# Kernel optimization log

Hardware: AMD Instinct MI355X
Metric: run time of the kernel (lower is better)

Reference implementation:

```python
import jax, jax.numpy as jnp
import numpy as np

SMALL = 1e-7
EPS = 1e-6


def setup_inputs() -> dict:
    key = jax.random.key(0)
    k1, k2 = jax.random.split(key)
    B, C, h, w = 8, 3, 1024, 1024
    src = jax.random.normal(k1, (B, C, h, w), dtype=jnp.float32)
    # near-identity homographies so warped coords land mostly in-bounds
    H = jnp.eye(3, dtype=jnp.float32)[None] + 0.05 * jax.random.normal(k2, (B, 3, 3), dtype=jnp.float32)
    return {"src": src, "H": H}


def reference(src, H):
    B, C, h, w = src.shape
    # homogeneous pixel grid: (3, h, w) = [x, y, 1]
    xx = jnp.arange(w, dtype=jnp.float32)
    yy = jnp.arange(h, dtype=jnp.float32)
    gx, gy = jnp.meshgrid(xx, yy)  # (h, w) each
    grid = jnp.stack([gx, gy, jnp.ones_like(gx)], axis=0)  # (3, h, w)

    # per-pixel homography transform: (B,3,h,w)
    warped = jnp.einsum('bij,jhw->bihw', H, grid)
    T = warped[:, 2]  # (B,h,w)
    T = T + EPS * (1.0 - (jnp.abs(T) >= SMALL).astype(jnp.float32))
    x = warped[:, 0] / T  # (B,h,w) source x-coords
    y = warped[:, 1] / T  # (B,h,w) source y-coords

    # bilinear sample with clamped corner indices (matches torch impl)
    x0 = jnp.floor(x).astype(jnp.int32)
    y0 = jnp.floor(y).astype(jnp.int32)
    x1 = jnp.clip(x0 + 1, 0, w - 1)
    y1 = jnp.clip(y0 + 1, 0, h - 1)
    x0 = jnp.clip(x0, 0, w - 1)
    y0 = jnp.clip(y0, 0, h - 1)

    im = jnp.transpose(src, (0, 2, 3, 1))  # (B,h,w,C)
    b = jnp.arange(B, dtype=jnp.int32)[:, None, None]  # (B,1,1)
    Ia = im[b, y0, x0]  # (B,h,w,C)
    Ib = im[b, y1, x0]
    Ic = im[b, y0, x1]
    Id = im[b, y1, x1]

    x0f, x1f = x0.astype(jnp.float32), x1.astype(jnp.float32)
    y0f, y1f = y0.astype(jnp.float32), y1.astype(jnp.float32)
    wa = ((x1f - x) * (y1f - y))[..., None]
    wb = ((x1f - x) * (y - y0f))[..., None]
    wc = ((x - x0f) * (y1f - y))[..., None]
    wd = ((x - x0f) * (y - y0f))[..., None]

    out = wa * Ia + wb * Ib + wc * Ic + wd * Id  # (B,h,w,C)
    return jnp.transpose(out, (0, 3, 1, 2))  # (B,C,h,w)
```

## Files before the change

kernel.cpp:

```cpp
#include <hip/hip_runtime.h>
#include <math.h>
#include <limits.h>
#include <string.h>


#define SMALL_F 1e-7f
#define EPS_F   1e-6f
#define PX 4

typedef float v2f __attribute__((ext_vector_type(2)));

__device__ __forceinline__ int cvt_f32_i32_x86(float f) {
    if (f >= 2147483648.0f) return INT_MIN;
    return (int)f;
}

__global__ void __launch_bounds__(256)
warp_bilinear_kernel(const float* __restrict__ src, const float* __restrict__ Hm,
                     float* __restrict__ out, int B, int h, int w) {
#pragma clang fp contract(off)
    const int b  = (int)blockIdx.y & 7;
    const int y  = (int)blockIdx.y >> 3;
    const int tx = threadIdx.x;
    const int xstart = blockIdx.x * (256 * PX) + tx;

    const float* Hb = Hm + (size_t)b * 9;
    const float H0 = Hb[0], H1 = Hb[1], H2 = Hb[2];
    const float H3 = Hb[3], H4 = Hb[4], H5 = Hb[5];
    const float H6 = Hb[6], H7 = Hb[7], H8 = Hb[8];
    const float gy = (float)y;
    const float p1 = H1 * gy, p4 = H4 * gy, p7 = H7 * gy;

    unsigned idx0[PX], idx1[PX];
    v2f wa2[2], wb2[2], wc2[2], wd2[2];
    bool sA[PX], sC[PX], valid[PX];
    bool allvalid = true;

#pragma unroll
    for (int j = 0; j < 2; ++j) {
        const int ka = 2 * j, kb = 2 * j + 1;
        const int xa = xstart + 256 * ka, xb_ = xstart + 256 * kb;
        valid[ka] = (xa < w); valid[kb] = (xb_ < w);
        allvalid &= valid[ka] & valid[kb];
        v2f gx = { (float)xa, (float)xb_ };
        v2f w0 = (H0 * gx + p1) + H2;
        v2f w1 = (H3 * gx + p4) + H5;
        v2f T  = (H6 * gx + p7) + H8;
        float Ta = T[0], Tb = T[1];
        if (!(fabsf(Ta) >= SMALL_F)) Ta = Ta + EPS_F;
        if (!(fabsf(Tb) >= SMALL_F)) Tb = Tb + EPS_F;
        v2f xs = { w0[0] / Ta, w0[1] / Tb };
        v2f ys = { w1[0] / Ta, w1[1] / Tb };

        v2f x0f, x1f, y0f, y1f;
#pragma unroll
        for (int e = 0; e < 2; ++e) {
            const int k = 2 * j + e;
            int x0u = cvt_f32_i32_x86(floorf(xs[e]));
            int y0u = cvt_f32_i32_x86(floorf(ys[e]));
            int x1 = min(max(x0u + 1, 0), w - 1);
            int y1 = min(max(y0u + 1, 0), h - 1);
            int x0 = min(max(x0u, 0), w - 1);
            int y0 = min(max(y0u, 0), h - 1);
            x0f[e] = (float)x0; x1f[e] = (float)x1;
            y0f[e] = (float)y0; y1f[e] = (float)y1;
            int xb = min(max(x0u, 0), w - 2);
            sA[k] = (x0 == xb);
            sC[k] = (x1 == xb);
            idx0[k] = (unsigned)(y0 * w + xb);
            idx1[k] = (unsigned)(y1 * w + xb);
        }
        v2f t1 = x1f - xs;
        v2f t2 = y1f - ys;
        v2f t3 = ys - y0f;
        v2f t4 = xs - x0f;
        wa2[j] = t1 * t2;
        wb2[j] = t1 * t3;
        wc2[j] = t4 * t2;
        wd2[j] = t4 * t3;
    }

    const size_t plane = (size_t)h * (size_t)w;
    const float* sb = src + (size_t)b * 3 * plane;
    float* ob = out + (size_t)b * 3 * plane + (size_t)y * (size_t)w;

    if (allvalid) {
        float q0[3][PX][2], q1[3][PX][2];
#pragma unroll
        for (int c = 0; c < 3; ++c) {
            const float* sc = sb + (size_t)c * plane;
#pragma unroll
            for (int k = 0; k < PX; ++k) {
                __builtin_memcpy(q0[c][k], sc + idx0[k], 8);
                __builtin_memcpy(q1[c][k], sc + idx1[k], 8);
            }
        }
#pragma unroll
        for (int c = 0; c < 3; ++c) {
            float* oc = ob + (size_t)c * plane;
#pragma unroll
            for (int j = 0; j < 2; ++j) {
                const int ka = 2 * j, kb = 2 * j + 1;
                v2f Ia = { sA[ka] ? q0[c][ka][0] : q0[c][ka][1],
                           sA[kb] ? q0[c][kb][0] : q0[c][kb][1] };
                v2f Ic = { sC[ka] ? q0[c][ka][0] : q0[c][ka][1],
                           sC[kb] ? q0[c][kb][0] : q0[c][kb][1] };
                v2f Ib = { sA[ka] ? q1[c][ka][0] : q1[c][ka][1],
                           sA[kb] ? q1[c][kb][0] : q1[c][kb][1] };
                v2f Id = { sC[ka] ? q1[c][ka][0] : q1[c][ka][1],
                           sC[kb] ? q1[c][kb][0] : q1[c][kb][1] };
                v2f r = ((wa2[j] * Ia + wb2[j] * Ib) + wc2[j] * Ic) + wd2[j] * Id;
                __builtin_nontemporal_store(r[0], oc + xstart + 256 * ka);
                __builtin_nontemporal_store(r[1], oc + xstart + 256 * kb);
            }
        }
    } else {
#pragma unroll
        for (int c = 0; c < 3; ++c) {
            const float* sc = sb + (size_t)c * plane;
            float* oc = ob + (size_t)c * plane;
#pragma unroll
            for (int k = 0; k < PX; ++k) {
                if (!valid[k]) continue;
                float pr0[2], pr1[2];
                __builtin_memcpy(pr0, sc + idx0[k], 8);
                __builtin_memcpy(pr1, sc + idx1[k], 8);
                float Ia = sA[k] ? pr0[0] : pr0[1];
                float Ic = sC[k] ? pr0[0] : pr0[1];
                float Ib = sA[k] ? pr1[0] : pr1[1];
                float Id = sC[k] ? pr1[0] : pr1[1];
                const int j = k >> 1, e = k & 1;
                float r = ((wa2[j][e] * Ia + wb2[j][e] * Ib) + wc2[j][e] * Ic)
                          + wd2[j][e] * Id;
                __builtin_nontemporal_store(r, oc + xstart + 256 * k);
            }
        }
    }
}

extern "C" void kernel_launch(void* const* d_in, const int* in_sizes, int n_in,
                              void* d_out, int out_size, void* d_ws, size_t ws_size,
                              hipStream_t stream) {
    const float* src = (const float*)d_in[0];
    const float* Hm  = (const float*)d_in[1];
    float* out = (float*)d_out;

    const int B = in_sizes[1] / 9;
    const int C = 3;
    const size_t plane = (size_t)in_sizes[0] / ((size_t)B * C);
    const int h = 1024;
    const int w = (int)(plane / h);

    dim3 block(256, 1, 1);
    dim3 grid((w + 256 * PX - 1) / (256 * PX), (unsigned)(B * h), 1);
    warp_bilinear_kernel<<<grid, block, 0, stream>>>(src, Hm, out, B, h, w);
}
```

Measured before the change: 191.0 us.

## Load and blend per channel, add occupancy hint, move batch to grid z

```diff
diff --git a/kernel.cpp b/kernel.cpp
--- a/kernel.cpp
+++ b/kernel.cpp
@@ -15,12 +15,12 @@
     return (int)f;
 }
 
-__global__ void __launch_bounds__(256)
+__global__ void __launch_bounds__(256, 8)
 warp_bilinear_kernel(const float* __restrict__ src, const float* __restrict__ Hm,
                      float* __restrict__ out, int B, int h, int w) {
 #pragma clang fp contract(off)
-    const int b  = (int)blockIdx.y & 7;
-    const int y  = (int)blockIdx.y >> 3;
+    const int y  = blockIdx.y;
+    const int b  = blockIdx.z;
     const int tx = threadIdx.x;
     const int xstart = blockIdx.x * (256 * PX) + tx;
 
@@ -34,14 +34,12 @@
     unsigned idx0[PX], idx1[PX];
     v2f wa2[2], wb2[2], wc2[2], wd2[2];
     bool sA[PX], sC[PX], valid[PX];
-    bool allvalid = true;
 
 #pragma unroll
     for (int j = 0; j < 2; ++j) {
         const int ka = 2 * j, kb = 2 * j + 1;
         const int xa = xstart + 256 * ka, xb_ = xstart + 256 * kb;
         valid[ka] = (xa < w); valid[kb] = (xb_ < w);
-        allvalid &= valid[ka] & valid[kb];
         v2f gx = { (float)xa, (float)xb_ };
         v2f w0 = (H0 * gx + p1) + H2;
         v2f w1 = (H3 * gx + p4) + H5;
@@ -84,31 +82,30 @@
     const float* sb = src + (size_t)b * 3 * plane;
     float* ob = out + (size_t)b * 3 * plane + (size_t)y * (size_t)w;
 
-    if (allvalid) {
-        float q0[3][PX][2], q1[3][PX][2];
+    const bool fullblock = ((blockIdx.x + 1) * (256 * PX)) <= (unsigned)w;
+
+    if (fullblock) {
 #pragma unroll
         for (int c = 0; c < 3; ++c) {
             const float* sc = sb + (size_t)c * plane;
+            float* oc = ob + (size_t)c * plane;
+            float q0[PX][2], q1[PX][2];
 #pragma unroll
             for (int k = 0; k < PX; ++k) {
-                __builtin_memcpy(q0[c][k], sc + idx0[k], 8);
-                __builtin_memcpy(q1[c][k], sc + idx1[k], 8);
+                __builtin_memcpy(q0[k], sc + idx0[k], 8);
+                __builtin_memcpy(q1[k], sc + idx1[k], 8);
             }
-        }
-#pragma unroll
-        for (int c = 0; c < 3; ++c) {
-            float* oc = ob + (size_t)c * plane;
 #pragma unroll
             for (int j = 0; j < 2; ++j) {
                 const int ka = 2 * j, kb = 2 * j + 1;
-                v2f Ia = { sA[ka] ? q0[c][ka][0] : q0[c][ka][1],
-                           sA[kb] ? q0[c][kb][0] : q0[c][kb][1] };
-                v2f Ic = { sC[ka] ? q0[c][ka][0] : q0[c][ka][1],
-                           sC[kb] ? q0[c][kb][0] : q0[c][kb][1] };
-                v2f Ib = { sA[ka] ? q1[c][ka][0] : q1[c][ka][1],
-                           sA[kb] ? q1[c][kb][0] : q1[c][kb][1] };
-                v2f Id = { sC[ka] ? q1[c][ka][0] : q1[c][ka][1],
-                           sC[kb] ? q1[c][kb][0] : q1[c][kb][1] };
+                v2f Ia = { sA[ka] ? q0[ka][0] : q0[ka][1],
+                           sA[kb] ? q0[kb][0] : q0[kb][1] };
+                v2f Ic = { sC[ka] ? q0[ka][0] : q0[ka][1],
+                           sC[kb] ? q0[kb][0] : q0[kb][1] };
+                v2f Ib = { sA[ka] ? q1[ka][0] : q1[ka][1],
+                           sA[kb] ? q1[kb][0] : q1[kb][1] };
+                v2f Id = { sC[ka] ? q1[ka][0] : q1[ka][1],
+                           sC[kb] ? q1[kb][0] : q1[kb][1] };
                 v2f r = ((wa2[j] * Ia + wb2[j] * Ib) + wc2[j] * Ic) + wd2[j] * Id;
                 __builtin_nontemporal_store(r[0], oc + xstart + 256 * ka);
                 __builtin_nontemporal_store(r[1], oc + xstart + 256 * kb);
@@ -152,6 +149,6 @@
     const int w = (int)(plane / h);
 
     dim3 block(256, 1, 1);
-    dim3 grid((w + 256 * PX - 1) / (256 * PX), (unsigned)(B * h), 1);
+    dim3 grid((w + 256 * PX - 1) / (256 * PX), h, B);
     warp_bilinear_kernel<<<grid, block, 0, stream>>>(src, Hm, out, B, h, w);
 }
```

After: 221.0 us. 1.16x slower.
